# Kernel optimization log

Measured on AMD Instinct MI355X. Metric: run time of the kernel, lower is better.

Reference implementation:

```python
import jax, jax.numpy as jnp
import numpy as np

D_MODEL = 1024
D_FF = 4096
NUM_EXPERTS = 8
TOP_K = 2
LB_COEF = 0.01
Z_COEF = 0.001
EPS_LN = 1e-5


def setup_inputs() -> dict:
    key = jax.random.key(0)
    ks = jax.random.split(key, 8)
    B, L = 4, 2048
    s_in = 1.0 / np.sqrt(D_MODEL)
    s_ff = 1.0 / np.sqrt(D_FF)
    return {
        "x": jax.random.normal(ks[0], (B, L, D_MODEL), dtype=jnp.float32),
        "gate_w": jax.random.normal(ks[1], (NUM_EXPERTS, D_MODEL), dtype=jnp.float32) * s_in,
        "ln_g": jnp.ones((D_MODEL,), dtype=jnp.float32),
        "ln_b": jnp.zeros((D_MODEL,), dtype=jnp.float32),
        "w1": jax.random.normal(ks[2], (NUM_EXPERTS, D_MODEL, D_FF), dtype=jnp.float32) * s_in,
        "b1": jnp.zeros((NUM_EXPERTS, D_FF), dtype=jnp.float32),
        "w2": jax.random.normal(ks[3], (NUM_EXPERTS, D_FF, D_MODEL), dtype=jnp.float32) * s_ff,
        "b2": jnp.zeros((NUM_EXPERTS, D_MODEL), dtype=jnp.float32),
    }


def reference(x, gate_w, ln_g, ln_b, w1, b1, w2, b2):
    B, L, D = x.shape
    xf = x.reshape(-1, D)  # [T, D]

    # LayerNorm
    mu = jnp.mean(xf, axis=-1, keepdims=True)
    var = jnp.mean((xf - mu) ** 2, axis=-1, keepdims=True)
    x_norm = (xf - mu) * jax.lax.rsqrt(var + EPS_LN) * ln_g + ln_b

    # Router (eval mode: no noise)
    logits = jnp.clip(x_norm @ gate_w.T, -10.0, 10.0)  # [T, E]
    z_loss = jnp.mean(jax.nn.logsumexp(logits, axis=-1) ** 2) * Z_COEF
    probs = jax.nn.softmax(logits, axis=-1)

    gw, idx = jax.lax.top_k(probs, TOP_K)  # [T, K]
    gw = gw / (jnp.sum(gw, axis=-1, keepdims=True) + 1e-8)

    # Load-balancing aux loss uses top-1 assignment
    top1_mask = jax.nn.one_hot(idx[:, 0], NUM_EXPERTS, dtype=jnp.float32)
    fraction_routed = jnp.mean(top1_mask, axis=0)
    mean_prob = jnp.mean(probs, axis=0)
    aux_loss = NUM_EXPERTS * jnp.sum(fraction_routed * mean_prob) * LB_COEF
    total_aux = aux_loss + z_loss

    # Combine weights [T, E]: sum over k of gate weight where routed to e
    combine = jnp.einsum("tk,tke->te", gw, jax.nn.one_hot(idx, NUM_EXPERTS, dtype=gw.dtype))

    # Dense per-expert FFN (Expert: Linear -> GELU -> Linear), combined by weights
    out = jnp.zeros_like(xf)
    for e in range(NUM_EXPERTS):
        h = jax.nn.gelu(x_norm @ w1[e] + b1[e], approximate=False)
        y = h @ w2[e] + b2[e]
        out = out + combine[:, e:e + 1] * y

    return x + out.reshape(B, L, D), total_aux
```

## Files before the change

kernel.cpp:

```cpp
#include <hip/hip_runtime.h>
#include <math.h>

typedef __bf16 bf16_t;
typedef bf16_t bf16x8 __attribute__((ext_vector_type(8)));
typedef bf16_t bf16x4 __attribute__((ext_vector_type(4)));
typedef float  f32x4  __attribute__((ext_vector_type(4)));

#define T_TOK 8192
#define DM 1024
#define DF 4096
#define NE 8
#define NP 16384

__device__ __forceinline__ f32x4 mfma_bf16(bf16x8 a, bf16x8 b, f32x4 c) {
  return __builtin_amdgcn_mfma_f32_16x16x32_bf16(a, b, c, 0, 0, 0);
}

__device__ __forceinline__ void gload16(const void* g, void* l) {
  __builtin_amdgcn_global_load_lds((const __attribute__((address_space(1))) void*)g,
                                   (__attribute__((address_space(3))) void*)l, 16, 0, 0);
}

__device__ __forceinline__ float erf_fast(float x) {
  float ax = fabsf(x);
  float t = 1.f / (1.f + 0.3275911f * ax);
  float p = t * (0.254829592f + t * (-0.284496736f + t * (1.421413741f +
            t * (-1.453152027f + t * 1.061405429f))));
  float r = 1.f - p * __expf(-ax * ax);
  return copysignf(r, x);
}

__device__ __forceinline__ unsigned swz_off(int row, int ch) {
  return (unsigned)(((row >> 1) << 7) + (((((row & 1) << 2) | ch) ^ ((row >> 1) & 7)) << 4));
}


__global__ __launch_bounds__(256) void k_router(
    const float* __restrict__ x, const float* __restrict__ gate_w,
    const float* __restrict__ ln_g, const float* __restrict__ ln_b,
    float* __restrict__ out, bf16_t* __restrict__ xn,
    int* __restrict__ eidx, float* __restrict__ gts, int* __restrict__ meta)
{
  int* cnt1 = meta;
  int* cnt2 = meta + 8;
  float* probsum = (float*)(meta + 32);
  float* zsum    = (float*)(meta + 40);

  __shared__ float sprob[8];
  __shared__ float sz;
  __shared__ int sc1[8], sc2[8];
  if (threadIdx.x < 8) { sprob[threadIdx.x] = 0.f; sc1[threadIdx.x] = 0; sc2[threadIdx.x] = 0; }
  if (threadIdx.x == 8) sz = 0.f;
  __syncthreads();

  int lane = threadIdx.x & 63, wv = threadIdx.x >> 6;
  int t = blockIdx.x * 4 + wv;
  const float* xt = x + (size_t)t * DM;

  float4 v[4];
  float s1 = 0.f, s2 = 0.f;
  #pragma unroll
  for (int c = 0; c < 4; ++c) {
    v[c] = *(const float4*)(xt + c * 256 + lane * 4);
    s1 += v[c].x + v[c].y + v[c].z + v[c].w;
    s2 += v[c].x * v[c].x + v[c].y * v[c].y + v[c].z * v[c].z + v[c].w * v[c].w;
  }
  #pragma unroll
  for (int o = 32; o > 0; o >>= 1) { s1 += __shfl_xor(s1, o, 64); s2 += __shfl_xor(s2, o, 64); }
  float mu = s1 * (1.f / DM);
  float var = s2 * (1.f / DM) - mu * mu;
  float rstd = rsqrtf(var + 1e-5f);

  float xv[16];
  #pragma unroll
  for (int c = 0; c < 4; ++c) {
    int d = c * 256 + lane * 4;
    float4 g4 = *(const float4*)(ln_g + d);
    float4 b4 = *(const float4*)(ln_b + d);
    xv[c*4+0] = (v[c].x - mu) * rstd * g4.x + b4.x;
    xv[c*4+1] = (v[c].y - mu) * rstd * g4.y + b4.y;
    xv[c*4+2] = (v[c].z - mu) * rstd * g4.z + b4.z;
    xv[c*4+3] = (v[c].w - mu) * rstd * g4.w + b4.w;
    *(float4*)(out + (size_t)t * DM + d) = v[c];
    bf16x4 pk = { (bf16_t)xv[c*4+0], (bf16_t)xv[c*4+1], (bf16_t)xv[c*4+2], (bf16_t)xv[c*4+3] };
    *(bf16x4*)(xn + (size_t)t * DM + d) = pk;
  }

  float lg[8];
  #pragma unroll
  for (int e = 0; e < 8; ++e) {
    float p = 0.f;
    #pragma unroll
    for (int c = 0; c < 4; ++c) {
      int d = c * 256 + lane * 4;
      float4 g4 = *(const float4*)(gate_w + e * DM + d);
      p += xv[c*4+0] * g4.x + xv[c*4+1] * g4.y + xv[c*4+2] * g4.z + xv[c*4+3] * g4.w;
    }
    #pragma unroll
    for (int o = 32; o > 0; o >>= 1) p += __shfl_xor(p, o, 64);
    lg[e] = p;
  }

  if (lane == 0) {
    float m = -1e30f;
    #pragma unroll
    for (int e = 0; e < 8; ++e) { lg[e] = fminf(fmaxf(lg[e], -10.f), 10.f); m = fmaxf(m, lg[e]); }
    float pr[8]; float se = 0.f;
    #pragma unroll
    for (int e = 0; e < 8; ++e) { pr[e] = expf(lg[e] - m); se += pr[e]; }
    float inv = 1.f / se;
    #pragma unroll
    for (int e = 0; e < 8; ++e) pr[e] *= inv;
    float lse = m + logf(se);

    int e0 = 0; float p0 = pr[0];
    #pragma unroll
    for (int e = 1; e < 8; ++e) if (pr[e] > p0) { p0 = pr[e]; e0 = e; }
    int e1 = -1; float p1 = -1.f;
    #pragma unroll
    for (int e = 0; e < 8; ++e) if (e != e0 && pr[e] > p1) { p1 = pr[e]; e1 = e; }
    float s = p0 + p1 + 1e-8f;
    eidx[t*2]   = e0; eidx[t*2+1] = e1;
    gts[t*2]    = p0 / s; gts[t*2+1] = p1 / s;

    atomicAdd(&sc1[e0], 1);
    atomicAdd(&sc2[e0], 1);
    atomicAdd(&sc2[e1], 1);
    #pragma unroll
    for (int e = 0; e < 8; ++e) atomicAdd(&sprob[e], pr[e]);
    atomicAdd(&sz, lse * lse);
  }
  __syncthreads();
  if (threadIdx.x < 8) {
    if (sc1[threadIdx.x]) atomicAdd(&cnt1[threadIdx.x], sc1[threadIdx.x]);
    if (sc2[threadIdx.x]) atomicAdd(&cnt2[threadIdx.x], sc2[threadIdx.x]);
    atomicAdd(&probsum[threadIdx.x], sprob[threadIdx.x]);
  }
  if (threadIdx.x == 8) atomicAdd(zsum, sz);
}

__global__ __launch_bounds__(256) void k_convT2(
    const float* __restrict__ w1, bf16_t* __restrict__ w1t,
    const float* __restrict__ w2, bf16_t* __restrict__ w2t)
{
  int bid = blockIdx.x;
  const float* s; bf16_t* d; int R, C, c0, r0;
  if (bid < 8192) {
    int e = bid >> 10, rem = bid & 1023;
    R = DM; C = DF;
    s = w1 + (size_t)e * R * C; d = w1t + (size_t)e * R * C;
    c0 = (rem & 63) * 64; r0 = (rem >> 6) * 64;
  } else {
    int e = (bid - 8192) >> 10, rem = (bid - 8192) & 1023;
    R = DF; C = DM;
    s = w2 + (size_t)e * R * C; d = w2t + (size_t)e * R * C;
    c0 = (rem & 15) * 64; r0 = (rem >> 4) * 64;
  }

  __shared__ float tile[64][65];
  int t = threadIdx.x;
  #pragma unroll
  for (int i = 0; i < 4; ++i) {
    int idx = i * 256 + t;
    int r = idx >> 4, c4 = (idx & 15) * 4;
    float4 v = *(const float4*)(s + (size_t)(r0 + r) * C + c0 + c4);
    tile[r][c4]   = v.x; tile[r][c4+1] = v.y;
    tile[r][c4+2] = v.z; tile[r][c4+3] = v.w;
  }
  __syncthreads();
  #pragma unroll
  for (int i = 0; i < 2; ++i) {
    int idx = i * 256 + t;
    int c = idx >> 3, r8 = (idx & 7) * 8;
    bf16x8 pk;
    #pragma unroll
    for (int k = 0; k < 8; ++k) pk[k] = (bf16_t)tile[r8 + k][c];
    *(bf16x8*)(d + (size_t)(c0 + c) * R + r0 + r8) = pk;
  }
}

__global__ void k_finalize(int* __restrict__ meta, float* __restrict__ aux_out) {
  if (threadIdx.x == 0 && blockIdx.x == 0) {
    int acc = 0;
    for (int e = 0; e < 8; ++e) { meta[24 + e] = acc; acc += meta[8 + e]; }
    const float* probsum = (const float*)(meta + 32);
    const float* zsum    = (const float*)(meta + 40);
    float s = 0.f;
    for (int e = 0; e < 8; ++e)
      s += ((float)meta[e] * (1.f / 8192.f)) * (probsum[e] * (1.f / 8192.f));
    aux_out[0] = 8.f * s * 0.01f + (zsum[0] * (1.f / 8192.f)) * 0.001f;
  }
}

__global__ __launch_bounds__(256) void k_assign(
    const int* __restrict__ eidx, float* __restrict__ gts,
    int* __restrict__ meta, int* __restrict__ list, float* __restrict__ gl,
    int* __restrict__ t2s)
{
  int t = blockIdx.x * 256 + threadIdx.x;
  int* cursor = meta + 16;
  const int* off = meta + 24;
  #pragma unroll
  for (int k = 0; k < 2; ++k) {
    int e = eidx[t*2 + k];
    float g = gts[t*2 + k];
    int pos = atomicAdd(&cursor[e], 1);
    int slot = off[e] + pos;
    list[slot] = t;
    gl[slot] = g;
    t2s[t*2 + k] = slot;
  }
}


#define VW(N) asm volatile("s_waitcnt vmcnt(" #N ")" ::: "memory")
#define BARSB do { __builtin_amdgcn_s_barrier(); __builtin_amdgcn_sched_barrier(0); } while (0)

#define STG_A(T, KS, P) do { \
  gload16(sAq[0] + (T)*64 + (KS)*32, smem + (P)*65536 + (KS)*16384 + dq[0]); \
  gload16(sAq[1] + (T)*64 + (KS)*32, smem + (P)*65536 + (KS)*16384 + dq[1]); } while (0)
#define STG_B(T, KS, P) do { \
  gload16(sBq[0] + (T)*64 + (KS)*32, smem + (P)*65536 + 32768 + (KS)*16384 + dq[0]); \
  gload16(sBq[1] + (T)*64 + (KS)*32, smem + (P)*65536 + 32768 + (KS)*16384 + dq[1]); } while (0)

#define LDA_(AF, P, KS) do { _Pragma("unroll") for (int i_ = 0; i_ < 8; ++i_) \
  AF[i_] = *(const bf16x8*)(smem + (P)*65536 + (KS)*16384 + a_off[i_]); } while (0)
#define LDBA(P, KS) do { \
  bfrA0 = *(const bf16x8*)(smem + (P)*65536 + 32768 + (KS)*16384 + b_off[0]); \
  bfrA1 = *(const bf16x8*)(smem + (P)*65536 + 32768 + (KS)*16384 + b_off[1]); } while (0)
#define LDBB(P, KS) do { \
  bfrB0 = *(const bf16x8*)(smem + (P)*65536 + 32768 + (KS)*16384 + b_off[2]); \
  bfrB1 = *(const bf16x8*)(smem + (P)*65536 + 32768 + (KS)*16384 + b_off[3]); } while (0)

#define FMAQ(AF, B0, B1, NH) do { __builtin_amdgcn_s_setprio(1); \
  _Pragma("unroll") for (int i_ = 0; i_ < 8; ++i_) { \
    acc[i_][(NH)*2+0] = mfma_bf16(AF[i_], B0, acc[i_][(NH)*2+0]); \
    acc[i_][(NH)*2+1] = mfma_bf16(AF[i_], B1, acc[i_][(NH)*2+1]); } \
  __builtin_amdgcn_s_setprio(0); } while (0)

#define TILE(T, P) do { \
  STG_A((T)+1, 0, (P)^1); VW(6); BARSB; \
  LDA_(afr0, P, 0); LDBA(P, 0); FMAQ(afr0, bfrA0, bfrA1, 0); \
  STG_B((T)+1, 0, (P)^1); VW(8); BARSB; \
  LDBB(P, 0); FMAQ(afr0, bfrB0, bfrB1, 1); \
  STG_A((T)+1, 1, (P)^1); VW(6); BARSB; \
  LDA_(afr1, P, 1); LDBA(P, 1); FMAQ(afr1, bfrA0, bfrA1, 0); \
  STG_B((T)+1, 1, (P)^1); VW(8); BARSB; \
  LDBB(P, 1); FMAQ(afr1, bfrB0, bfrB1, 1); \
} while (0)

#define TAIL(P) do { \
  VW(4); BARSB; LDA_(afr0, P, 0); LDBA(P, 0); FMAQ(afr0, bfrA0, bfrA1, 0); \
  VW(4); BARSB; LDBB(P, 0); FMAQ(afr0, bfrB0, bfrB1, 1); \
  VW(0); BARSB; LDA_(afr1, P, 1); LDBA(P, 1); FMAQ(afr1, bfrA0, bfrA1, 0); \
  VW(0); BARSB; LDBB(P, 1); FMAQ(afr1, bfrB0, bfrB1, 1); \
} while (0)

#define GEMM_PIPE(NT) do { \
  STG_A(0, 0, 0); STG_B(0, 0, 0); STG_A(0, 1, 0); STG_B(0, 1, 0); \
  for (int t_ = 0; t_ + 2 < (NT); t_ += 2) { TILE(t_, 0); TILE(t_ + 1, 1); } \
  TILE((NT) - 2, 0); \
  TAIL(1); \
} while (0)

__global__ __launch_bounds__(512, 1) void k_ffn1(
    const bf16_t* __restrict__ xn, const bf16_t* __restrict__ w1t,
    const float* __restrict__ b1, bf16_t* __restrict__ H,
    const int* __restrict__ list, const int* __restrict__ meta)
{
  extern __shared__ char smem[];
  int bid = blockIdx.x;
  int xcd = bid & 7, idx = bid >> 3;
  int m = idx & 31, pn = idx >> 5;
  int g = pn * 8 + xcd;
  int e = g >> 4, n = g & 15;

  int cnt = meta[8 + e];
  int m0 = m * 256;
  if (m0 >= cnt) return;
  int offe = meta[24 + e];
  int n0 = n * 256;

  int tid = threadIdx.x, lane = tid & 63, wv = tid >> 6;
  int wm = wv >> 2, wn = wv & 3;

  const bf16_t* sAq[2]; const bf16_t* sBq[2];
  unsigned dq[2];
  #pragma unroll
  for (int i = 0; i < 2; ++i) {
    int s = i * 512 + tid;
    int line = s >> 3, u = s & 7, w = u ^ (line & 7);
    int row = (line << 1) | (w >> 2), ch = w & 3;
    int mrow = min(m0 + row, cnt - 1);
    int token = list[offe + mrow];
    sAq[i] = xn + (size_t)token * DM + ch * 8;
    sBq[i] = w1t + ((size_t)e * DF + n0 + row) * DM + ch * 8;
    dq[i] = (unsigned)(i * 8192 + wv * 1024);
  }

  unsigned a_off[8], b_off[4];
  #pragma unroll
  for (int i = 0; i < 8; ++i) a_off[i] = swz_off(wm * 128 + i * 16 + (lane & 15), lane >> 4);
  #pragma unroll
  for (int j = 0; j < 4; ++j)
    b_off[j] = swz_off(wn * 64 + (j >> 1) * 32 + (j & 1) * 16 + (lane & 15), lane >> 4);

  f32x4 acc[8][4];
  #pragma unroll
  for (int i = 0; i < 8; ++i)
    #pragma unroll
    for (int j = 0; j < 4; ++j)
      acc[i][j] = (f32x4){0.f, 0.f, 0.f, 0.f};
  bf16x8 afr0[8], afr1[8], bfrA0, bfrA1, bfrB0, bfrB1;

  GEMM_PIPE(DM / 64);

  __syncthreads();
  unsigned wbase = (unsigned)(wv * 18432);
  int rq = (lane >> 4) << 2;
  #pragma unroll
  for (int i = 0; i < 8; ++i) {
    #pragma unroll
    for (int j = 0; j < 4; ++j) {
      int colL = (j >> 1) * 32 + (j & 1) * 16 + (lane & 15);
      float bb = b1[e * DF + n0 + wn * 64 + colL];
      #pragma unroll
      for (int q = 0; q < 4; ++q) {
        int rowL = i * 16 + rq + q;
        float hv = acc[i][j][q] + bb;
        hv = 0.5f * hv * (1.f + erf_fast(hv * 0.70710678118f));
        *(bf16_t*)(smem + wbase + rowL * 144 + colL * 2) = (bf16_t)hv;
      }
    }
  }
  __syncthreads();
  #pragma unroll
  for (int it = 0; it < 16; ++it) {
    int slot = it * 64 + lane;
    int rowL = slot >> 3, chunk = slot & 7;
    int mg = m0 + wm * 128 + rowL;
    if (mg < cnt) {
      bf16x8 vv = *(const bf16x8*)(smem + wbase + rowL * 144 + chunk * 16);
      *(bf16x8*)(&H[(size_t)(offe + mg) * DF + n0 + wn * 64 + chunk * 8]) = vv;
    }
  }
}

__global__ __launch_bounds__(512, 1) void k_ffn2(
    const bf16_t* __restrict__ H, const bf16_t* __restrict__ w2t,
    const float* __restrict__ b2, bf16_t* __restrict__ Y,
    const int* __restrict__ meta)
{
  extern __shared__ char smem[];
  int bid = blockIdx.x;
  int xcd = bid & 7, idx = bid >> 3;
  int m = idx & 31, pn = idx >> 5;
  int g = pn * 8 + xcd;
  int e = g >> 2, n = g & 3;

  int cnt = meta[8 + e];
  int m0 = m * 256;
  if (m0 >= cnt) return;
  int offe = meta[24 + e];
  int n0 = n * 256;

  int tid = threadIdx.x, lane = tid & 63, wv = tid >> 6;
  int wm = wv >> 2, wn = wv & 3;

  const bf16_t* sAq[2]; const bf16_t* sBq[2];
  unsigned dq[2];
  #pragma unroll
  for (int i = 0; i < 2; ++i) {
    int s = i * 512 + tid;
    int line = s >> 3, u = s & 7, w = u ^ (line & 7);
    int row = (line << 1) | (w >> 2), ch = w & 3;
    int mrow = min(m0 + row, cnt - 1);
    sAq[i] = H + (size_t)(offe + mrow) * DF + ch * 8;
    sBq[i] = w2t + ((size_t)e * DM + n0 + row) * DF + ch * 8;
    dq[i] = (unsigned)(i * 8192 + wv * 1024);
  }

  unsigned a_off[8], b_off[4];
  #pragma unroll
  for (int i = 0; i < 8; ++i) a_off[i] = swz_off(wm * 128 + i * 16 + (lane & 15), lane >> 4);
  #pragma unroll
  for (int j = 0; j < 4; ++j)
    b_off[j] = swz_off(wn * 64 + (j >> 1) * 32 + (j & 1) * 16 + (lane & 15), lane >> 4);

  f32x4 acc[8][4];
  #pragma unroll
  for (int i = 0; i < 8; ++i)
    #pragma unroll
    for (int j = 0; j < 4; ++j)
      acc[i][j] = (f32x4){0.f, 0.f, 0.f, 0.f};
  bf16x8 afr0[8], afr1[8], bfrA0, bfrA1, bfrB0, bfrB1;

  GEMM_PIPE(DF / 64);

  __syncthreads();
  unsigned wbase = (unsigned)(wv * 18432);
  int rq = (lane >> 4) << 2;
  #pragma unroll
  for (int i = 0; i < 8; ++i) {
    #pragma unroll
    for (int j = 0; j < 4; ++j) {
      int colL = (j >> 1) * 32 + (j & 1) * 16 + (lane & 15);
      float bb = b2[e * DM + n0 + wn * 64 + colL];
      #pragma unroll
      for (int q = 0; q < 4; ++q) {
        int rowL = i * 16 + rq + q;
        *(bf16_t*)(smem + wbase + rowL * 144 + colL * 2) = (bf16_t)(acc[i][j][q] + bb);
      }
    }
  }
  __syncthreads();
  #pragma unroll
  for (int it = 0; it < 16; ++it) {
    int slot = it * 64 + lane;
    int rowL = slot >> 3, chunk = slot & 7;
    int mg = m0 + wm * 128 + rowL;
    if (mg < cnt) {
      bf16x8 vv = *(const bf16x8*)(smem + wbase + rowL * 144 + chunk * 16);
      *(bf16x8*)(&Y[(size_t)(offe + mg) * DM + n0 + wn * 64 + chunk * 8]) = vv;
    }
  }
}

__global__ __launch_bounds__(256) void k_combine(
    const bf16_t* __restrict__ Y, const int* __restrict__ t2s,
    const float* __restrict__ gl, float* __restrict__ out)
{
  int lane = threadIdx.x & 63, wv = threadIdx.x >> 6;
  int t = blockIdx.x * 4 + wv;
  int s0 = t2s[t*2], s1 = t2s[t*2 + 1];
  float g0 = gl[s0], g1 = gl[s1];
  const bf16_t* y0 = Y + (size_t)s0 * DM;
  const bf16_t* y1 = Y + (size_t)s1 * DM;
  float* o = out + (size_t)t * DM;
  #pragma unroll
  for (int c = 0; c < 4; ++c) {
    int d = c * 256 + lane * 4;
    float4 r  = *(const float4*)(o + d);
    bf16x4 a = *(const bf16x4*)(y0 + d);
    bf16x4 b = *(const bf16x4*)(y1 + d);
    r.x += g0 * (float)a[0] + g1 * (float)b[0];
    r.y += g0 * (float)a[1] + g1 * (float)b[1];
    r.z += g0 * (float)a[2] + g1 * (float)b[2];
    r.w += g0 * (float)a[3] + g1 * (float)b[3];
    *(float4*)(o + d) = r;
  }
}

extern "C" void kernel_launch(void* const* d_in, const int* in_sizes, int n_in,
                              void* d_out, int out_size, void* d_ws, size_t ws_size,
                              hipStream_t stream) {
  const float* x      = (const float*)d_in[0];
  const float* gate_w = (const float*)d_in[1];
  const float* ln_g   = (const float*)d_in[2];
  const float* ln_b   = (const float*)d_in[3];
  const float* w1     = (const float*)d_in[4];
  const float* b1     = (const float*)d_in[5];
  const float* w2     = (const float*)d_in[6];
  const float* b2     = (const float*)d_in[7];
  float* out = (float*)d_out;

  char* ws = (char*)d_ws;
  bf16_t* xn   = (bf16_t*)(ws);
  bf16_t* w1t  = (bf16_t*)(ws + 16777216ull);
  bf16_t* Y    = (bf16_t*)(ws + 16777216ull);
  bf16_t* w2t  = (bf16_t*)(ws + 83886080ull);
  bf16_t* H    = (bf16_t*)(ws + 150994944ull);
  int*    list = (int*)   (ws + 285212672ull);
  float*  gl   = (float*) (ws + 285278208ull);
  int*    eidx = (int*)   (ws + 285343744ull);
  float*  gts  = (float*) (ws + 285409280ull);
  int*    t2s  = (int*)   (ws + 285409280ull);
  int*    meta = (int*)   (ws + 285474816ull);

  hipFuncSetAttribute((const void*)k_ffn1, hipFuncAttributeMaxDynamicSharedMemorySize, 147456);
  hipFuncSetAttribute((const void*)k_ffn2, hipFuncAttributeMaxDynamicSharedMemorySize, 147456);

  hipMemsetAsync(meta, 0, 256, stream);
  k_router<<<T_TOK / 4, 256, 0, stream>>>(x, gate_w, ln_g, ln_b, out, xn, eidx, gts, meta);
  k_convT2<<<16384, 256, 0, stream>>>(w1, w1t, w2, w2t);
  k_finalize<<<1, 1, 0, stream>>>(meta, out + (size_t)T_TOK * DM);
  k_assign<<<T_TOK / 256, 256, 0, stream>>>(eidx, gts, meta, list, gl, t2s);
  k_ffn1<<<NE * 16 * 32, 512, 147456, stream>>>(xn, w1t, b1, H, list, meta);
  k_ffn2<<<NE * 4 * 32, 512, 147456, stream>>>(H, w2t, b2, Y, meta);
  k_combine<<<T_TOK / 4, 256, 0, stream>>>(Y, t2s, gl, out);
}
```

Measured before the change: 658.7 us.

## Reorder GEMM pipeline barriers and switch FFN grids to 3D launch

The double-buffered GEMM loop now issues its LDS fragment reads before staging the next tile's global-to-LDS loads. Compute steps are bracketed with plain s_barriers, and the old sched_barrier fences are dropped, changing where the vmcnt waits fall. Both FFN kernels also drop the XCD-aware block-index swizzle and use a plain dim3(n, m, expert) grid. The intent is to overlap loads with MFMA differently and simplify indexing. The cost is twice as many barriers per tile and possible loss of L2 locality across XCDs.

```diff
diff --git a/kernel.cpp b/kernel.cpp
--- a/kernel.cpp
+++ b/kernel.cpp
@@ -213,8 +213,8 @@
 }
 
 
+#define BAR __builtin_amdgcn_s_barrier()
 #define VW(N) asm volatile("s_waitcnt vmcnt(" #N ")" ::: "memory")
-#define BARSB do { __builtin_amdgcn_s_barrier(); __builtin_amdgcn_sched_barrier(0); } while (0)
 
 #define STG_A(T, KS, P) do { \
   gload16(sAq[0] + (T)*64 + (KS)*32, smem + (P)*65536 + (KS)*16384 + dq[0]); \
@@ -239,25 +239,26 @@
   __builtin_amdgcn_s_setprio(0); } while (0)
 
 #define TILE(T, P) do { \
-  STG_A((T)+1, 0, (P)^1); VW(6); BARSB; \
-  LDA_(afr0, P, 0); LDBA(P, 0); FMAQ(afr0, bfrA0, bfrA1, 0); \
-  STG_B((T)+1, 0, (P)^1); VW(8); BARSB; \
-  LDBB(P, 0); FMAQ(afr0, bfrB0, bfrB1, 1); \
-  STG_A((T)+1, 1, (P)^1); VW(6); BARSB; \
-  LDA_(afr1, P, 1); LDBA(P, 1); FMAQ(afr1, bfrA0, bfrA1, 0); \
-  STG_B((T)+1, 1, (P)^1); VW(8); BARSB; \
-  LDBB(P, 1); FMAQ(afr1, bfrB0, bfrB1, 1); \
+  LDA_(afr0, P, 0); LDBA(P, 0); STG_A((T)+1, 0, (P)^1); BAR; \
+  FMAQ(afr0, bfrA0, bfrA1, 0); BAR; \
+  LDBB(P, 0); STG_B((T)+1, 0, (P)^1); VW(4); BAR; \
+  FMAQ(afr0, bfrB0, bfrB1, 1); BAR; \
+  LDA_(afr1, P, 1); LDBA(P, 1); STG_A((T)+1, 1, (P)^1); BAR; \
+  FMAQ(afr1, bfrA0, bfrA1, 0); BAR; \
+  LDBB(P, 1); STG_B((T)+1, 1, (P)^1); VW(4); BAR; \
+  FMAQ(afr1, bfrB0, bfrB1, 1); BAR; \
 } while (0)
 
 #define TAIL(P) do { \
-  VW(4); BARSB; LDA_(afr0, P, 0); LDBA(P, 0); FMAQ(afr0, bfrA0, bfrA1, 0); \
-  VW(4); BARSB; LDBB(P, 0); FMAQ(afr0, bfrB0, bfrB1, 1); \
-  VW(0); BARSB; LDA_(afr1, P, 1); LDBA(P, 1); FMAQ(afr1, bfrA0, bfrA1, 0); \
-  VW(0); BARSB; LDBB(P, 1); FMAQ(afr1, bfrB0, bfrB1, 1); \
+  LDA_(afr0, P, 0); LDBA(P, 0); BAR; FMAQ(afr0, bfrA0, bfrA1, 0); BAR; \
+  LDBB(P, 0); VW(0); BAR; FMAQ(afr0, bfrB0, bfrB1, 1); BAR; \
+  LDA_(afr1, P, 1); LDBA(P, 1); BAR; FMAQ(afr1, bfrA0, bfrA1, 0); BAR; \
+  LDBB(P, 1); BAR; FMAQ(afr1, bfrB0, bfrB1, 1); BAR; \
 } while (0)
 
 #define GEMM_PIPE(NT) do { \
   STG_A(0, 0, 0); STG_B(0, 0, 0); STG_A(0, 1, 0); STG_B(0, 1, 0); \
+  VW(4); BAR; \
   for (int t_ = 0; t_ + 2 < (NT); t_ += 2) { TILE(t_, 0); TILE(t_ + 1, 1); } \
   TILE((NT) - 2, 0); \
   TAIL(1); \
@@ -269,17 +270,12 @@
     const int* __restrict__ list, const int* __restrict__ meta)
 {
   extern __shared__ char smem[];
-  int bid = blockIdx.x;
-  int xcd = bid & 7, idx = bid >> 3;
-  int m = idx & 31, pn = idx >> 5;
-  int g = pn * 8 + xcd;
-  int e = g >> 4, n = g & 15;
-
+  int e = blockIdx.z;
   int cnt = meta[8 + e];
-  int m0 = m * 256;
+  int m0 = blockIdx.y * 256;
   if (m0 >= cnt) return;
   int offe = meta[24 + e];
-  int n0 = n * 256;
+  int n0 = blockIdx.x * 256;
 
   int tid = threadIdx.x, lane = tid & 63, wv = tid >> 6;
   int wm = wv >> 2, wn = wv & 3;
@@ -352,17 +348,12 @@
     const int* __restrict__ meta)
 {
   extern __shared__ char smem[];
-  int bid = blockIdx.x;
-  int xcd = bid & 7, idx = bid >> 3;
-  int m = idx & 31, pn = idx >> 5;
-  int g = pn * 8 + xcd;
-  int e = g >> 2, n = g & 3;
-
+  int e = blockIdx.z;
   int cnt = meta[8 + e];
-  int m0 = m * 256;
+  int m0 = blockIdx.y * 256;
   if (m0 >= cnt) return;
   int offe = meta[24 + e];
-  int n0 = n * 256;
+  int n0 = blockIdx.x * 256;
 
   int tid = threadIdx.x, lane = tid & 63, wv = tid >> 6;
   int wm = wv >> 2, wn = wv & 3;
@@ -485,7 +476,7 @@
   k_convT2<<<16384, 256, 0, stream>>>(w1, w1t, w2, w2t);
   k_finalize<<<1, 1, 0, stream>>>(meta, out + (size_t)T_TOK * DM);
   k_assign<<<T_TOK / 256, 256, 0, stream>>>(eidx, gts, meta, list, gl, t2s);
-  k_ffn1<<<NE * 16 * 32, 512, 147456, stream>>>(xn, w1t, b1, H, list, meta);
-  k_ffn2<<<NE * 4 * 32, 512, 147456, stream>>>(H, w2t, b2, Y, meta);
+  k_ffn1<<<dim3(DF / 256, 32, NE), 512, 147456, stream>>>(xn, w1t, b1, H, list, meta);
+  k_ffn2<<<dim3(DM / 256, 32, NE), 512, 147456, stream>>>(H, w2t, b2, Y, meta);
   k_combine<<<T_TOK / 4, 256, 0, stream>>>(Y, t2s, gl, out);
 }
```

Result: no change. 670.9 us (+1.9%).
